# Optimization experiments

Measured on AMD Instinct MI355X. Metric: run time of the kernel, lower is better.

## Reference

```python
import jax, jax.numpy as jnp
import numpy as np

HEADS = 12
D_MODEL = 768
D_TOKEN = D_MODEL // HEADS


def setup_inputs() -> dict:
    key = jax.random.key(0)
    ks = jax.random.split(key, 11)
    B, S, D = 2, 4096, D_MODEL
    scale = 1.0 / np.sqrt(D)
    return {
        "q": jax.random.normal(ks[0], (B, S, D), jnp.float32),
        "k": jax.random.normal(ks[1], (B, S, D), jnp.float32),
        "v": jax.random.normal(ks[2], (B, S, D), jnp.float32),
        "Wq": jax.random.normal(ks[3], (D, D), jnp.float32) * scale,
        "bq": jnp.zeros((D,), jnp.float32),
        "Wk": jax.random.normal(ks[4], (D, D), jnp.float32) * scale,
        "bk": jnp.zeros((D,), jnp.float32),
        "Wv": jax.random.normal(ks[5], (D, D), jnp.float32) * scale,
        "bv": jnp.zeros((D,), jnp.float32),
        "Wo": jax.random.normal(ks[6], (D, D), jnp.float32) * scale,
        "bo": jnp.zeros((D,), jnp.float32),
    }


def reference(q, k, v, Wq, bq, Wk, bk, Wv, bv, Wo, bo):
    B, S, D = q.shape
    H, Dh = HEADS, D_TOKEN
    # Linear projections (torch Linear: x @ W.T + b), split into heads: [B,H,S,Dh]
    qh = (q @ Wq.T + bq).reshape(B, S, H, Dh).transpose(0, 2, 1, 3)
    kh = (k @ Wk.T + bk).reshape(B, S, H, Dh).transpose(0, 2, 1, 3)
    vh = (v @ Wv.T + bv).reshape(B, S, H, Dh).transpose(0, 2, 1, 3)
    # Scaled dot-product attention (full O(S^2) scores, as the original does)
    scores = jnp.einsum("bhqd,bhkd->bhqk", qh, kh) / jnp.sqrt(
        jnp.asarray(Dh, qh.dtype))
    attn = jax.nn.softmax(scores, axis=-1)
    ctx = jnp.einsum("bhqk,bhkd->bhqd", attn, vh)
    ctx = ctx.transpose(0, 2, 1, 3).reshape(B, S, D)
    return ctx @ Wo.T + bo
```

## Files before the change

### kernel.cpp

```cpp
#include <hip/hip_runtime.h>


typedef __attribute__((ext_vector_type(4))) float f32x4;
typedef __attribute__((ext_vector_type(16))) float f32x16;
typedef __attribute__((ext_vector_type(8))) __bf16 bf16x8;
typedef __attribute__((ext_vector_type(2))) int i32x2;
typedef __attribute__((ext_vector_type(4))) unsigned u32x4;
using u16 = unsigned short;
using u32 = unsigned;

__device__ __forceinline__ u16 f2bf(float x) {
  __bf16 h = (__bf16)x;
  return __builtin_bit_cast(u16, h);
}
__device__ __forceinline__ float bf2f(u16 h) {
  return __uint_as_float(((unsigned)h) << 16);
}
__device__ __forceinline__ u32 pk2(float lo, float hi) {
  u32 r;
  asm("v_cvt_pk_bf16_f32 %0, %1, %2" : "=v"(r) : "v"(lo), "v"(hi));
  return r;
}
__device__ __forceinline__ void gload16(u16* ldsDst, const u16* gSrc) {
  __builtin_amdgcn_global_load_lds(
      (const __attribute__((address_space(1))) void*)gSrc,
      (__attribute__((address_space(3))) void*)ldsDst, 16, 0, 0);
}
__device__ __forceinline__ f32x4 mfma16(bf16x8 a, bf16x8 b, f32x4 c) {
  return __builtin_amdgcn_mfma_f32_16x16x32_bf16(a, b, c, 0, 0, 0);
}
__device__ __forceinline__ f32x16 mfma32(bf16x8 a, bf16x8 b, f32x16 c) {
  return __builtin_amdgcn_mfma_f32_32x32x16_bf16(a, b, c, 0, 0, 0);
}
__device__ __forceinline__ bf16x8 ld8(const u16* p) { return *(const bf16x8*)p; }

__global__ void cvt_hi(const float4* __restrict__ in0, u16* o0,
                       const float4* __restrict__ in1, u16* o1,
                       const float4* __restrict__ in2, u16* o2, int n4) {
  const float4* in = in0; u16* o = o0;
  if (blockIdx.y == 1) { in = in1; o = o1; }
  else if (blockIdx.y == 2) { in = in2; o = o2; }
  const int stride = gridDim.x * blockDim.x;
  for (int i = blockIdx.x * blockDim.x + threadIdx.x; i < n4; i += stride) {
    float4 x = in[i];
    *(ushort4*)&o[i * 4] = make_ushort4(f2bf(x.x), f2bf(x.y), f2bf(x.z), f2bf(x.w));
  }
}

__global__ void cvt_split(const float4* __restrict__ in0, u16* h0, u16* l0,
                          const float4* __restrict__ in1, u16* h1, u16* l1,
                          const float4* __restrict__ in2, u16* h2, u16* l2,
                          const float4* __restrict__ in3, u16* h3, u16* l3,
                          int n4) {
  const float4* in = in0; u16* hi = h0; u16* lo = l0;
  if (blockIdx.y == 1) { in = in1; hi = h1; lo = l1; }
  else if (blockIdx.y == 2) { in = in2; hi = h2; lo = l2; }
  else if (blockIdx.y == 3) { in = in3; hi = h3; lo = l3; }
  const int stride = gridDim.x * blockDim.x;
  for (int i = blockIdx.x * blockDim.x + threadIdx.x; i < n4; i += stride) {
    float4 x = in[i];
    float xs[4] = {x.x, x.y, x.z, x.w};
    u16 hh[4], ll[4];
#pragma unroll
    for (int j = 0; j < 4; ++j) {
      hh[j] = f2bf(xs[j]);
      ll[j] = f2bf(xs[j] - bf2f(hh[j]));
    }
    *(ushort4*)&hi[i * 4] = make_ushort4(hh[0], hh[1], hh[2], hh[3]);
    *(ushort4*)&lo[i * 4] = make_ushort4(ll[0], ll[1], ll[2], ll[3]);
  }
}

__global__ __launch_bounds__(256, 2) void gemm_qkv(
    const u16* __restrict__ Aq, const u16* __restrict__ Ak, const u16* __restrict__ Av,
    const u16* __restrict__ wqh, const u16* __restrict__ wql,
    const u16* __restrict__ wkh, const u16* __restrict__ wkl,
    const u16* __restrict__ wvh, const u16* __restrict__ wvl,
    const float* __restrict__ bq, const float* __restrict__ bk,
    const float* __restrict__ bv,
    u16* __restrict__ oq, u16* __restrict__ ok, u16* __restrict__ ov,
    float qscale) {
  constexpr int K = 768;
  constexpr int BUF = 12288;
  __shared__ u16 lds[2 * BUF];
  const int z = blockIdx.z;
  const u16* A = (z == 0) ? Aq : (z == 1) ? Ak : Av;
  const u16* Bh = (z == 0) ? wqh : (z == 1) ? wkh : wvh;
  const u16* Bl = (z == 0) ? wql : (z == 1) ? wkl : wvl;
  const float* bias = (z == 0) ? bq : (z == 1) ? bk : bv;
  u16* C = (z == 0) ? oq : (z == 1) ? ok : ov;
  const float scale = (z == 0) ? qscale : 1.f;
  const bool vmode = (z == 2);

  const int tid = threadIdx.x, lane = tid & 63, w = tid >> 6;
  const int wr = w >> 1, wc = w & 1;
  const int g = lane >> 4, la = lane & 15;
  const int m0 = blockIdx.x * 128, n0 = blockIdx.y * 128;

  f32x4 acc[4][4] = {};

  auto stage = [&](int buf, int kt) {
    const int k0 = kt * 32;
#pragma unroll
    for (int j = 0; j < 2; ++j) {
      const int t = w * 2 + j;
      const int s = t * 64 + lane;
      const int sr = s >> 3, ph = s & 7, ch = ph ^ (sr & 7);
      const int row = sr * 2 + (ch >> 2), c = ch & 3;
      const int gofs = k0 + c * 8;
      u16* base = &lds[buf * BUF];
      gload16(base + t * 512, A + (size_t)(m0 + row) * K + gofs);
      gload16(base + 4096 + t * 512, Bh + (size_t)(n0 + row) * K + gofs);
      gload16(base + 8192 + t * 512, Bl + (size_t)(n0 + row) * K + gofs);
    }
  };
  auto rdfrag = [&](const u16* base, int row, int c) -> bf16x8 {
    const int sr = row >> 1;
    const int ph = (((row & 1) << 2) | c) ^ (sr & 7);
    return ld8(base + sr * 64 + ph * 8);
  };

  stage(0, 0);
  __syncthreads();
  constexpr int nk = K / 32;
  int cur = 0;
  for (int kt = 0; kt < nk; ++kt) {
    if (kt + 1 < nk) stage(cur ^ 1, kt + 1);
    const u16* bA = &lds[cur * BUF];
    bf16x8 aH[4], bH[4], bL[4];
#pragma unroll
    for (int mi = 0; mi < 4; ++mi) aH[mi] = rdfrag(bA, wr * 64 + mi * 16 + la, g);
#pragma unroll
    for (int ni = 0; ni < 4; ++ni) {
      bH[ni] = rdfrag(bA + 4096, wc * 64 + ni * 16 + la, g);
      bL[ni] = rdfrag(bA + 8192, wc * 64 + ni * 16 + la, g);
    }
#pragma unroll
    for (int mi = 0; mi < 4; ++mi)
#pragma unroll
      for (int ni = 0; ni < 4; ++ni) {
        acc[mi][ni] = mfma16(aH[mi], bH[ni], acc[mi][ni]);
        acc[mi][ni] = mfma16(aH[mi], bL[ni], acc[mi][ni]);
      }
    __syncthreads();
    cur ^= 1;
  }

#pragma unroll
  for (int mi = 0; mi < 4; ++mi) {
    const int mbase = m0 + wr * 64 + mi * 16 + g * 4;
#pragma unroll
    for (int ni = 0; ni < 4; ++ni) {
      const int n = n0 + wc * 64 + ni * 16 + la;
      const float bv_ = bias[n];
#pragma unroll
      for (int r = 0; r < 4; ++r) {
        const int m = mbase + r;
        const float y = (acc[mi][ni][r] + bv_) * scale;
        const int bb = m >> 12, s = m & 4095, hh = n >> 6, dh = n & 63;
        if (!vmode)
          C[((size_t)(bb * 12 + hh) * 4096 + s) * 64 + dh] = f2bf(y);
        else
          C[((size_t)(bb * 12 + hh) * 64 + dh) * 4096 + s] = f2bf(y);
      }
    }
  }
}

__global__ __launch_bounds__(256, 2) void gemm_out(
    const u16* __restrict__ A, const u16* __restrict__ Bh,
    const float* __restrict__ bias, float* __restrict__ Cf) {
  constexpr int K = 768, N = 768;
  constexpr int BUF = 8192;
  __shared__ u16 lds[2 * BUF];
  const int tid = threadIdx.x, lane = tid & 63, w = tid >> 6;
  const int wr = w >> 1, wc = w & 1;
  const int g = lane >> 4, la = lane & 15;
  const int m0 = blockIdx.x * 128, n0 = blockIdx.y * 128;

  f32x4 acc[4][4] = {};

  auto stage = [&](int buf, int kt) {
    const int k0 = kt * 32;
#pragma unroll
    for (int j = 0; j < 2; ++j) {
      const int t = w * 2 + j;
      const int s = t * 64 + lane;
      const int sr = s >> 3, ph = s & 7, ch = ph ^ (sr & 7);
      const int row = sr * 2 + (ch >> 2), c = ch & 3;
      const int gofs = k0 + c * 8;
      u16* base = &lds[buf * BUF];
      gload16(base + t * 512, A + (size_t)(m0 + row) * K + gofs);
      gload16(base + 4096 + t * 512, Bh + (size_t)(n0 + row) * K + gofs);
    }
  };
  auto rdfrag = [&](const u16* base, int row, int c) -> bf16x8 {
    const int sr = row >> 1;
    const int ph = (((row & 1) << 2) | c) ^ (sr & 7);
    return ld8(base + sr * 64 + ph * 8);
  };

  stage(0, 0);
  __syncthreads();
  constexpr int nk = K / 32;
  int cur = 0;
  for (int kt = 0; kt < nk; ++kt) {
    if (kt + 1 < nk) stage(cur ^ 1, kt + 1);
    const u16* bA = &lds[cur * BUF];
    bf16x8 aH[4], bH[4];
#pragma unroll
    for (int mi = 0; mi < 4; ++mi) aH[mi] = rdfrag(bA, wr * 64 + mi * 16 + la, g);
#pragma unroll
    for (int ni = 0; ni < 4; ++ni) bH[ni] = rdfrag(bA + 4096, wc * 64 + ni * 16 + la, g);
#pragma unroll
    for (int mi = 0; mi < 4; ++mi)
#pragma unroll
      for (int ni = 0; ni < 4; ++ni)
        acc[mi][ni] = mfma16(aH[mi], bH[ni], acc[mi][ni]);
    __syncthreads();
    cur ^= 1;
  }

#pragma unroll
  for (int mi = 0; mi < 4; ++mi) {
    const int mbase = m0 + wr * 64 + mi * 16 + g * 4;
#pragma unroll
    for (int ni = 0; ni < 4; ++ni) {
      const int n = n0 + wc * 64 + ni * 16 + la;
      const float bv_ = bias[n];
#pragma unroll
      for (int r = 0; r < 4; ++r)
        Cf[(size_t)(mbase + r) * N + n] = acc[mi][ni][r] + bv_;
    }
  }
}

__global__ __launch_bounds__(256, 3) void flash_attn(
    const u16* __restrict__ Q, const u16* __restrict__ Kt,
    const u16* __restrict__ Vt, u16* __restrict__ ctx) {
  __shared__ u16 lds[2 * 8192];
  const int tid = threadIdx.x, lane = tid & 63, w = tid >> 6;
  const int l5 = lane & 31, hi = lane >> 5;
  const int bh = blockIdx.y, b = bh / 12, h = bh % 12;
  const int q0 = blockIdx.x * 128 + w * 32;
  const size_t kbase = (size_t)bh * 4096 * 64;
  const size_t vbase = (size_t)bh * 64 * 4096;

  bf16x8 aQ[4];
#pragma unroll
  for (int ks = 0; ks < 4; ++ks)
    aQ[ks] = ld8(Q + kbase + (size_t)(q0 + l5) * 64 + ks * 16 + hi * 8);

  f32x16 accO0 = {}, accO1 = {}, accLP = {};
  f32x16 M4;
#pragma unroll
  for (int i = 0; i < 16; ++i) M4[i] = -4.0f;
  const u32x4 onebits = {0x3F803F80u, 0x3F803F80u, 0x3F803F80u, 0x3F803F80u};
  const bf16x8 ones = __builtin_bit_cast(bf16x8, onebits);

  int aK0[4], aK1[4];
  {
    const int r0 = l5, f0 = (r0 & 7) ^ (r0 >> 3);
    const int r1 = 32 + l5, f1 = (r1 & 7) ^ (r1 >> 3);
#pragma unroll
    for (int ks = 0; ks < 4; ++ks) {
      aK0[ks] = r0 * 64 + (((ks * 2 + hi) ^ f0) << 3);
      aK1[ks] = r1 * 64 + (((ks * 2 + hi) ^ f1) << 3);
    }
  }

  const u16 *gk0, *gk1, *gv0, *gv1;
  int dK0, dK1, dV0, dV1;
  {
    const int t0 = w * 2, s0_ = t0 * 64 + lane;
    const int sr0 = s0_ >> 3, c0 = (s0_ & 7) ^ ((sr0 & 7) ^ (sr0 >> 3));
    gk0 = Kt + kbase + (size_t)sr0 * 64 + c0 * 8;
    gv0 = Vt + vbase + (size_t)sr0 * 4096 + c0 * 8;
    dK0 = t0 * 512; dV0 = 4096 + t0 * 512;
    const int t1 = t0 + 1, s1_ = t1 * 64 + lane;
    const int sr1 = s1_ >> 3, c1 = (s1_ & 7) ^ ((sr1 & 7) ^ (sr1 >> 3));
    gk1 = Kt + kbase + (size_t)sr1 * 64 + c1 * 8;
    gv1 = Vt + vbase + (size_t)sr1 * 4096 + c1 * 8;
    dK1 = t1 * 512; dV1 = 4096 + t1 * 512;
  }

  auto stage = [&](int bufbase, int tile) {
    gload16(&lds[bufbase + dK0], gk0 + (size_t)tile * 4096);
    gload16(&lds[bufbase + dK1], gk1 + (size_t)tile * 4096);
    gload16(&lds[bufbase + dV0], gv0 + tile * 64);
    gload16(&lds[bufbase + dV1], gv1 + tile * 64);
  };

  auto body = [&](const int B0) {
    f32x16 s0, s1;
    {
      bf16x8 k0 = ld8(&lds[B0 + aK0[0]]);
      bf16x8 k1 = ld8(&lds[B0 + aK1[0]]);
      s0 = mfma32(k0, aQ[0], M4);
      s1 = mfma32(k1, aQ[0], M4);
    }
#pragma unroll
    for (int ks = 1; ks < 4; ++ks) {
      bf16x8 k0 = ld8(&lds[B0 + aK0[ks]]);
      bf16x8 k1 = ld8(&lds[B0 + aK1[ks]]);
      s0 = mfma32(k0, aQ[ks], s0);
      s1 = mfma32(k1, aQ[ks], s1);
    }
#pragma unroll
    for (int ct = 0; ct < 2; ++ct) {
      const f32x16 sv = ct ? s1 : s0;
      float p[16];
#pragma unroll
      for (int i = 0; i < 16; ++i) p[i] = __builtin_exp2f(sv[i]);
      u32 W[4][2];
#pragma unroll
      for (int qd = 0; qd < 4; ++qd) {
        W[qd][0] = pk2(p[qd * 4 + 0], p[qd * 4 + 1]);
        W[qd][1] = pk2(p[qd * 4 + 2], p[qd * 4 + 3]);
      }
#pragma unroll
      for (int s2 = 0; s2 < 2; ++s2) {
        i32x2 r1 = __builtin_amdgcn_permlane32_swap((int)W[2 * s2][0], (int)W[2 * s2 + 1][0], false, false);
        i32x2 r2 = __builtin_amdgcn_permlane32_swap((int)W[2 * s2][1], (int)W[2 * s2 + 1][1], false, false);
        u32x4 wq = {(u32)r1.x, (u32)r2.x, (u32)r1.y, (u32)r2.y};
        const bf16x8 pb = __builtin_bit_cast(bf16x8, wq);
        const int ksv = ct * 2 + s2;
        bf16x8 v0 = ld8(&lds[B0 + 4096 + aK0[ksv]]);
        bf16x8 v1 = ld8(&lds[B0 + 4096 + aK1[ksv]]);
        accO0 = mfma32(v0, pb, accO0);
        accO1 = mfma32(v1, pb, accO1);
        accLP = mfma32(ones, pb, accLP);
      }
    }
  };

  stage(0, 0);
  __syncthreads();
#pragma unroll 1
  for (int t2 = 0; t2 < 32; ++t2) {
    stage(8192, 2 * t2 + 1);
    body(0);
    __syncthreads();
    if (t2 < 31) stage(0, 2 * t2 + 2);
    body(8192);
    __syncthreads();
  }

  const float inv = __builtin_amdgcn_rcpf(accLP[0]);
  u16* crow = ctx + ((size_t)b * 4096 + q0 + l5) * 768 + h * 64;
#pragma unroll
  for (int dt = 0; dt < 2; ++dt) {
    const f32x16 a = dt ? accO1 : accO0;
#pragma unroll
    for (int rq = 0; rq < 4; ++rq) {
      const int d0 = dt * 32 + 8 * rq + 4 * hi;
      uint2 st;
      st.x = pk2(a[rq * 4 + 0] * inv, a[rq * 4 + 1] * inv);
      st.y = pk2(a[rq * 4 + 2] * inv, a[rq * 4 + 3] * inv);
      *(uint2*)&crow[d0] = st;
    }
  }
}

extern "C" void kernel_launch(void* const* d_in, const int* in_sizes, int n_in,
                              void* d_out, int out_size, void* d_ws, size_t ws_size,
                              hipStream_t stream) {
  constexpr int NQKV = 2 * 4096 * 768;
  constexpr int NW = 768 * 768;
  const float* q = (const float*)d_in[0];
  const float* k = (const float*)d_in[1];
  const float* v = (const float*)d_in[2];
  const float* Wq = (const float*)d_in[3];
  const float* bq = (const float*)d_in[4];
  const float* Wk = (const float*)d_in[5];
  const float* bk = (const float*)d_in[6];
  const float* Wv = (const float*)d_in[7];
  const float* bv = (const float*)d_in[8];
  const float* Wo = (const float*)d_in[9];
  const float* bo = (const float*)d_in[10];

  char* p = (char*)d_ws;
  auto take = [&](size_t n) -> u16* {
    u16* r = (u16*)p;
    p += (n * 2 + 255) & ~(size_t)255;
    return r;
  };
  u16 *q_h = take(NQKV), *k_h = take(NQKV), *v_h = take(NQKV);
  u16 *wq_h = take(NW), *wq_l = take(NW);
  u16 *wk_h = take(NW), *wk_l = take(NW);
  u16 *wv_h = take(NW), *wv_l = take(NW);
  u16 *wo_h = take(NW), *wo_l = take(NW);
  u16 *qh = take(NQKV), *kh = take(NQKV), *vt = take(NQKV), *ctx = take(NQKV);

  cvt_hi<<<dim3(1024, 3), 256, 0, stream>>>(
      (const float4*)q, q_h, (const float4*)k, k_h, (const float4*)v, v_h, NQKV / 4);
  cvt_split<<<dim3(288, 4), 256, 0, stream>>>(
      (const float4*)Wq, wq_h, wq_l, (const float4*)Wk, wk_h, wk_l,
      (const float4*)Wv, wv_h, wv_l, (const float4*)Wo, wo_h, wo_l, NW / 4);

  const float qscale = 0.18033688011112042f;
  gemm_qkv<<<dim3(64, 6, 3), 256, 0, stream>>>(
      q_h, k_h, v_h, wq_h, wq_l, wk_h, wk_l, wv_h, wv_l,
      bq, bk, bv, qh, kh, vt, qscale);
  flash_attn<<<dim3(32, 24), 256, 0, stream>>>(qh, kh, vt, ctx);
  gemm_out<<<dim3(64, 6), 256, 0, stream>>>(ctx, wo_h, bo, (float*)d_out);
}
```

Measured before the change: 259.9 us.

## Process two query tiles per wave in flash attention, sum row totals on VALU

The attention kernel now runs 2 waves per block, and each wave handles 64 queries as two 32-row tiles. Each K/V fragment read from LDS therefore feeds two MFMAs, and each thread issues four K and four V async loads per stage. The softmax denominator is now accumulated with VALU adds and a cross-half shuffle, replacing the extra ones-vector MFMA. The constant -4 exponent offset is also dropped, since it cancels in the normalization. In exchange, the kernel has half as many resident waves, uses more registers per wave and has less latency hiding.

New measurement: 281.0 us. 1.08x slower.

```diff
diff --git a/kernel.cpp b/kernel.cpp
--- a/kernel.cpp
+++ b/kernel.cpp
@@ -235,28 +235,27 @@
   }
 }
 
-__global__ __launch_bounds__(256, 3) void flash_attn(
+__global__ __launch_bounds__(128, 2) void flash_attn(
     const u16* __restrict__ Q, const u16* __restrict__ Kt,
     const u16* __restrict__ Vt, u16* __restrict__ ctx) {
   __shared__ u16 lds[2 * 8192];
   const int tid = threadIdx.x, lane = tid & 63, w = tid >> 6;
   const int l5 = lane & 31, hi = lane >> 5;
   const int bh = blockIdx.y, b = bh / 12, h = bh % 12;
-  const int q0 = blockIdx.x * 128 + w * 32;
+  const int q0 = blockIdx.x * 128 + w * 64;
   const size_t kbase = (size_t)bh * 4096 * 64;
   const size_t vbase = (size_t)bh * 64 * 4096;
 
-  bf16x8 aQ[4];
-#pragma unroll
-  for (int ks = 0; ks < 4; ++ks)
-    aQ[ks] = ld8(Q + kbase + (size_t)(q0 + l5) * 64 + ks * 16 + hi * 8);
-
-  f32x16 accO0 = {}, accO1 = {}, accLP = {};
-  f32x16 M4;
-#pragma unroll
-  for (int i = 0; i < 16; ++i) M4[i] = -4.0f;
-  const u32x4 onebits = {0x3F803F80u, 0x3F803F80u, 0x3F803F80u, 0x3F803F80u};
-  const bf16x8 ones = __builtin_bit_cast(bf16x8, onebits);
+  bf16x8 aQA[4], aQB[4];
+#pragma unroll
+  for (int ks = 0; ks < 4; ++ks) {
+    aQA[ks] = ld8(Q + kbase + (size_t)(q0 + l5) * 64 + ks * 16 + hi * 8);
+    aQB[ks] = ld8(Q + kbase + (size_t)(q0 + 32 + l5) * 64 + ks * 16 + hi * 8);
+  }
+
+  f32x16 oA0 = {}, oA1 = {}, oB0 = {}, oB1 = {};
+  f32x16 z16 = {};
+  float lpA = 0.f, lpB = 0.f;
 
   int aK0[4], aK1[4];
   {
@@ -269,67 +268,85 @@
     }
   }
 
-  const u16 *gk0, *gk1, *gv0, *gv1;
-  int dK0, dK1, dV0, dV1;
-  {
-    const int t0 = w * 2, s0_ = t0 * 64 + lane;
-    const int sr0 = s0_ >> 3, c0 = (s0_ & 7) ^ ((sr0 & 7) ^ (sr0 >> 3));
-    gk0 = Kt + kbase + (size_t)sr0 * 64 + c0 * 8;
-    gv0 = Vt + vbase + (size_t)sr0 * 4096 + c0 * 8;
-    dK0 = t0 * 512; dV0 = 4096 + t0 * 512;
-    const int t1 = t0 + 1, s1_ = t1 * 64 + lane;
-    const int sr1 = s1_ >> 3, c1 = (s1_ & 7) ^ ((sr1 & 7) ^ (sr1 >> 3));
-    gk1 = Kt + kbase + (size_t)sr1 * 64 + c1 * 8;
-    gv1 = Vt + vbase + (size_t)sr1 * 4096 + c1 * 8;
-    dK1 = t1 * 512; dV1 = 4096 + t1 * 512;
-  }
-
-  auto stage = [&](int bufbase, int tile) {
-    gload16(&lds[bufbase + dK0], gk0 + (size_t)tile * 4096);
-    gload16(&lds[bufbase + dK1], gk1 + (size_t)tile * 4096);
-    gload16(&lds[bufbase + dV0], gv0 + tile * 64);
-    gload16(&lds[bufbase + dV1], gv1 + tile * 64);
+  const u16 *gk[4], *gv[4];
+  int dK[4], dV[4];
+#pragma unroll
+  for (int j = 0; j < 4; ++j) {
+    const int t = w * 4 + j;
+    const int sr = t * 8 + (lane >> 3);
+    const int c = (lane & 7) ^ (lane >> 3) ^ t;
+    gk[j] = Kt + kbase + (size_t)sr * 64 + c * 8;
+    gv[j] = Vt + vbase + (size_t)sr * 4096 + c * 8;
+    dK[j] = t * 512;
+    dV[j] = 4096 + t * 512;
+  }
+
+  auto stage = [&](int B0, int tile) {
+#pragma unroll
+    for (int j = 0; j < 4; ++j) {
+      gload16(&lds[B0 + dK[j]], gk[j] + (size_t)tile * 4096);
+      gload16(&lds[B0 + dV[j]], gv[j] + tile * 64);
+    }
   };
 
   auto body = [&](const int B0) {
-    f32x16 s0, s1;
+    f32x16 sA0, sA1, sB0, sB1;
     {
       bf16x8 k0 = ld8(&lds[B0 + aK0[0]]);
       bf16x8 k1 = ld8(&lds[B0 + aK1[0]]);
-      s0 = mfma32(k0, aQ[0], M4);
-      s1 = mfma32(k1, aQ[0], M4);
+      sA0 = mfma32(k0, aQA[0], z16);
+      sA1 = mfma32(k1, aQA[0], z16);
+      sB0 = mfma32(k0, aQB[0], z16);
+      sB1 = mfma32(k1, aQB[0], z16);
     }
 #pragma unroll
     for (int ks = 1; ks < 4; ++ks) {
       bf16x8 k0 = ld8(&lds[B0 + aK0[ks]]);
       bf16x8 k1 = ld8(&lds[B0 + aK1[ks]]);
-      s0 = mfma32(k0, aQ[ks], s0);
-      s1 = mfma32(k1, aQ[ks], s1);
+      sA0 = mfma32(k0, aQA[ks], sA0);
+      sA1 = mfma32(k1, aQA[ks], sA1);
+      sB0 = mfma32(k0, aQB[ks], sB0);
+      sB1 = mfma32(k1, aQB[ks], sB1);
     }
 #pragma unroll
     for (int ct = 0; ct < 2; ++ct) {
-      const f32x16 sv = ct ? s1 : s0;
-      float p[16];
-#pragma unroll
-      for (int i = 0; i < 16; ++i) p[i] = __builtin_exp2f(sv[i]);
-      u32 W[4][2];
+      const f32x16 svA = ct ? sA1 : sA0;
+      const f32x16 svB = ct ? sB1 : sB0;
+      u32 WA[4][2], WB[4][2];
 #pragma unroll
       for (int qd = 0; qd < 4; ++qd) {
-        W[qd][0] = pk2(p[qd * 4 + 0], p[qd * 4 + 1]);
-        W[qd][1] = pk2(p[qd * 4 + 2], p[qd * 4 + 3]);
+        const float a0 = __builtin_exp2f(svA[qd * 4 + 0]);
+        const float a1 = __builtin_exp2f(svA[qd * 4 + 1]);
+        const float a2 = __builtin_exp2f(svA[qd * 4 + 2]);
+        const float a3 = __builtin_exp2f(svA[qd * 4 + 3]);
+        lpA += (a0 + a1) + (a2 + a3);
+        WA[qd][0] = pk2(a0, a1);
+        WA[qd][1] = pk2(a2, a3);
+        const float b0 = __builtin_exp2f(svB[qd * 4 + 0]);
+        const float b1 = __builtin_exp2f(svB[qd * 4 + 1]);
+        const float b2 = __builtin_exp2f(svB[qd * 4 + 2]);
+        const float b3 = __builtin_exp2f(svB[qd * 4 + 3]);
+        lpB += (b0 + b1) + (b2 + b3);
+        WB[qd][0] = pk2(b0, b1);
+        WB[qd][1] = pk2(b2, b3);
       }
 #pragma unroll
       for (int s2 = 0; s2 < 2; ++s2) {
-        i32x2 r1 = __builtin_amdgcn_permlane32_swap((int)W[2 * s2][0], (int)W[2 * s2 + 1][0], false, false);
-        i32x2 r2 = __builtin_amdgcn_permlane32_swap((int)W[2 * s2][1], (int)W[2 * s2 + 1][1], false, false);
-        u32x4 wq = {(u32)r1.x, (u32)r2.x, (u32)r1.y, (u32)r2.y};
-        const bf16x8 pb = __builtin_bit_cast(bf16x8, wq);
+        i32x2 rA1 = __builtin_amdgcn_permlane32_swap((int)WA[2 * s2][0], (int)WA[2 * s2 + 1][0], false, false);
+        i32x2 rA2 = __builtin_amdgcn_permlane32_swap((int)WA[2 * s2][1], (int)WA[2 * s2 + 1][1], false, false);
+        u32x4 wqA = {(u32)rA1.x, (u32)rA2.x, (u32)rA1.y, (u32)rA2.y};
+        const bf16x8 pbA = __builtin_bit_cast(bf16x8, wqA);
+        i32x2 rB1 = __builtin_amdgcn_permlane32_swap((int)WB[2 * s2][0], (int)WB[2 * s2 + 1][0], false, false);
+        i32x2 rB2 = __builtin_amdgcn_permlane32_swap((int)WB[2 * s2][1], (int)WB[2 * s2 + 1][1], false, false);
+        u32x4 wqB = {(u32)rB1.x, (u32)rB2.x, (u32)rB1.y, (u32)rB2.y};
+        const bf16x8 pbB = __builtin_bit_cast(bf16x8, wqB);
         const int ksv = ct * 2 + s2;
         bf16x8 v0 = ld8(&lds[B0 + 4096 + aK0[ksv]]);
         bf16x8 v1 = ld8(&lds[B0 + 4096 + aK1[ksv]]);
-        accO0 = mfma32(v0, pb, accO0);
-        accO1 = mfma32(v1, pb, accO1);
-        accLP = mfma32(ones, pb, accLP);
+        oA0 = mfma32(v0, pbA, oA0);
+        oA1 = mfma32(v1, pbA, oA1);
+        oB0 = mfma32(v0, pbB, oB0);
+        oB1 = mfma32(v1, pbB, oB1);
       }
     }
   };
@@ -346,18 +363,26 @@
     __syncthreads();
   }
 
-  const float inv = __builtin_amdgcn_rcpf(accLP[0]);
-  u16* crow = ctx + ((size_t)b * 4096 + q0 + l5) * 768 + h * 64;
+  lpA += __shfl_xor(lpA, 32);
+  lpB += __shfl_xor(lpB, 32);
+  const float invA = __builtin_amdgcn_rcpf(lpA);
+  const float invB = __builtin_amdgcn_rcpf(lpB);
+  u16* crowA = ctx + ((size_t)b * 4096 + q0 + l5) * 768 + h * 64;
+  u16* crowB = crowA + (size_t)32 * 768;
 #pragma unroll
   for (int dt = 0; dt < 2; ++dt) {
-    const f32x16 a = dt ? accO1 : accO0;
+    const f32x16 a = dt ? oA1 : oA0;
+    const f32x16 c = dt ? oB1 : oB0;
 #pragma unroll
     for (int rq = 0; rq < 4; ++rq) {
       const int d0 = dt * 32 + 8 * rq + 4 * hi;
-      uint2 st;
-      st.x = pk2(a[rq * 4 + 0] * inv, a[rq * 4 + 1] * inv);
-      st.y = pk2(a[rq * 4 + 2] * inv, a[rq * 4 + 3] * inv);
-      *(uint2*)&crow[d0] = st;
+      uint2 stA, stB;
+      stA.x = pk2(a[rq * 4 + 0] * invA, a[rq * 4 + 1] * invA);
+      stA.y = pk2(a[rq * 4 + 2] * invA, a[rq * 4 + 3] * invA);
+      stB.x = pk2(c[rq * 4 + 0] * invB, c[rq * 4 + 1] * invB);
+      stB.y = pk2(c[rq * 4 + 2] * invB, c[rq * 4 + 3] * invB);
+      *(uint2*)&crowA[d0] = stA;
+      *(uint2*)&crowB[d0] = stB;
     }
   }
 }
@@ -402,6 +427,6 @@
   gemm_qkv<<<dim3(64, 6, 3), 256, 0, stream>>>(
       q_h, k_h, v_h, wq_h, wq_l, wk_h, wk_l, wv_h, wv_l,
       bq, bk, bv, qh, kh, vt, qscale);
-  flash_attn<<<dim3(32, 24), 256, 0, stream>>>(qh, kh, vt, ctx);
+  flash_attn<<<dim3(32, 24), 128, 0, stream>>>(qh, kh, vt, ctx);
   gemm_out<<<dim3(64, 6), 256, 0, stream>>>(ctx, wo_h, bo, (float*)d_out);
 }
```
